# Performance work log

Hardware: AMD Instinct MI355X
Metric: run time of the kernel (lower is better)

Reference implementation:

```python
import jax, jax.numpy as jnp
import numpy as np

KD, KY, KX = 3, 3, 3  # kernel_size from init_kwargs


def setup_inputs() -> dict:
    key = jax.random.key(0)
    x = jax.random.normal(key, (4, 2, 64, 256, 256), dtype=jnp.float32)
    return {"x": x}


def reference(x):
    # x: [B, CH, D, H, W]
    B, CH, D, H, W = x.shape
    pd, py, px = (KD - 1) // 2, (KY - 1) // 2, (KX - 1) // 2
    # replicate padding (torch F.pad mode='replicate' == jnp.pad mode='edge')
    xp = jnp.pad(x, ((0, 0), (0, 0), (pd, pd), (py, py), (px, px)), mode='edge')
    center = (KD * KY * KX) // 2  # flattened center position, excluded from max
    # running max over the 26 non-center neighbors; never materializes the
    # [B, CH, 27, D, H, W] tensor the torch conv3d path creates.
    max_nc = jnp.full(x.shape, -jnp.inf, dtype=x.dtype)
    idx = 0
    for i in range(KD):
        for j in range(KY):
            for k in range(KX):
                if idx != center:
                    shifted = xp[:, :, i:i + D, j:j + H, k:k + W]
                    max_nc = jnp.maximum(max_nc, shifted)
                idx += 1
    mask = x > max_nc  # strict local maximum (excluding self)
    return x * mask.astype(x.dtype)
```

## Files before the change

kernel.cpp:

```cpp
#include <hip/hip_runtime.h>


constexpr int D_   = 64;
constexpr int H_   = 256;
constexpr int W_   = 256;
constexpr int HW_  = H_ * W_;
constexpr int NVOL = 8;
constexpr int DC   = 8;
constexpr int RY   = 8;
constexpr int RS   = RY + 2;
constexpr int NBUF = 3;
constexpr int S    = DC + 2;

__device__ __forceinline__ float f3(float a, float b, float c) {
    return fmaxf(fmaxf(a, b), c);
}

__device__ __forceinline__ void gload16(const float* g, float* l) {
    __builtin_amdgcn_global_load_lds(
        (const __attribute__((address_space(1))) void*)g,
        (__attribute__((address_space(3))) void*)l,
        16, 0, 0);
}

__global__ __launch_bounds__(512, 6)
void nms3d(const float* __restrict__ x, float* __restrict__ out)
{
    __shared__ float lds[NBUF][RS * W_];

    const int tx = threadIdx.x;
    const int ty = threadIdx.y;
    const int h0 = blockIdx.y * RY;
    const int h  = h0 + ty;
    const int n  = blockIdx.z;
    const int z0 = blockIdx.x * DC;
    const int c  = tx << 2;

    const float* __restrict__ base  = x   + (size_t)n * D_ * HW_;
    float* __restrict__       obase = out + (size_t)n * D_ * HW_;

    const int grA = min(max(h0 - 1 + ty, 0), H_ - 1);
    const int grB = min(max(h0 - 1 + RY + ty, 0), H_ - 1);
    const float* gA = base + (size_t)grA * W_ + c;
    const float* gB = base + (size_t)grB * W_ + c;

    auto stage = [&](int t) {
        const int zc = min(max(z0 - 1 + t, 0), D_ - 1);
        const size_t zo = (size_t)zc * HW_;
        float* lp = &lds[t % NBUF][0];
        gload16(gA + zo, lp + ty * W_);
        if (ty < 2) gload16(gB + zo, lp + (RY + ty) * W_);
    };

    stage(0);

    float4 vm9_pp = {0,0,0,0};
    float4 vm9_p  = {0,0,0,0};
    float4 cr8_p  = {0,0,0,0};
    float4 vprev  = {0,0,0,0};

#pragma unroll
    for (int t = 0; t < S; ++t) {
        if (t + 1 < S) {
            stage(t + 1);
            if (ty < 2) asm volatile("s_waitcnt vmcnt(2)" ::: "memory");
            else        asm volatile("s_waitcnt vmcnt(1)" ::: "memory");
        } else {
            asm volatile("s_waitcnt vmcnt(0)" ::: "memory");
        }
        __builtin_amdgcn_s_barrier();
        asm volatile("" ::: "memory");

        const float* p = &lds[t % NBUF][0];
        const float4 a0 = *(const float4*)(p + (ty    ) * W_ + c);
        const float4 b0 = *(const float4*)(p + (ty + 1) * W_ + c);
        const float4 d0 = *(const float4*)(p + (ty + 2) * W_ + c);

        float4 va;
        va.x = fmaxf(a0.x, d0.x); va.y = fmaxf(a0.y, d0.y);
        va.z = fmaxf(a0.z, d0.z); va.w = fmaxf(a0.w, d0.w);

        float vaL = __shfl_up(va.w, 1);   if (tx == 0)  vaL = va.x;
        float vaR = __shfl_down(va.x, 1); if (tx == 63) vaR = va.w;
        float bL  = __shfl_up(b0.w, 1);   if (tx == 0)  bL  = b0.x;
        float bR  = __shfl_down(b0.x, 1); if (tx == 63) bR  = b0.w;

        float4 hv, nb;
        hv.x = f3(vaL, va.x, va.y);  hv.y = f3(va.x, va.y, va.z);
        hv.z = f3(va.y, va.z, va.w); hv.w = f3(va.z, va.w, vaR);
        nb.x = fmaxf(bL,  b0.y);  nb.y = fmaxf(b0.x, b0.z);
        nb.z = fmaxf(b0.y, b0.w); nb.w = fmaxf(b0.z, bR);

        float4 c8, cur;
        c8.x  = fmaxf(hv.x, nb.x); c8.y  = fmaxf(hv.y, nb.y);
        c8.z  = fmaxf(hv.z, nb.z); c8.w  = fmaxf(hv.w, nb.w);
        cur.x = fmaxf(c8.x, b0.x); cur.y = fmaxf(c8.y, b0.y);
        cur.z = fmaxf(c8.z, b0.z); cur.w = fmaxf(c8.w, b0.w);

        if (t >= 2) {
            const int zi = z0 - 1 + t;
            float4 mx, o;
            mx.x = f3(vm9_pp.x, cr8_p.x, cur.x);
            mx.y = f3(vm9_pp.y, cr8_p.y, cur.y);
            mx.z = f3(vm9_pp.z, cr8_p.z, cur.z);
            mx.w = f3(vm9_pp.w, cr8_p.w, cur.w);
            o.x = vprev.x > mx.x ? vprev.x : 0.0f;
            o.y = vprev.y > mx.y ? vprev.y : 0.0f;
            o.z = vprev.z > mx.z ? vprev.z : 0.0f;
            o.w = vprev.w > mx.w ? vprev.w : 0.0f;
            *(float4*)(obase + (size_t)(zi - 1) * HW_ + (size_t)h * W_ + c) = o;
        }
        vm9_pp = vm9_p; vm9_p = cur; cr8_p = c8; vprev = b0;
    }
}

extern "C" void kernel_launch(void* const* d_in, const int* in_sizes, int n_in,
                              void* d_out, int out_size, void* d_ws, size_t ws_size,
                              hipStream_t stream)
{
    const float* x = (const float*)d_in[0];
    float* out = (float*)d_out;
    dim3 block(64, RY, 1);
    dim3 grid(D_ / DC, H_ / RY, NVOL);
    nms3d<<<grid, block, 0, stream>>>(x, out);
}
```

Baseline: 233.4 us.

## Deepen LDS prefetch pipeline, enlarge depth chunk, and flatten block mapping

Each block now processes 16 depth slices instead of 8, which cuts how often halo slices are re-read across blocks. LDS rises to 4 buffers and loads are issued two slices ahead, with per-iteration vmcnt waits adjusted to match. The 3D grid becomes a 1D grid with the volume index varying fastest, and the launch bounds hint rises to 8 blocks. The risks are the hand-counted waitcnt schedule, which must also account for outstanding stores, and fewer blocks overall, which means less parallelism per CU.

```diff
diff --git a/kernel.cpp b/kernel.cpp
--- a/kernel.cpp
+++ b/kernel.cpp
@@ -6,10 +6,10 @@
 constexpr int W_   = 256;
 constexpr int HW_  = H_ * W_;
 constexpr int NVOL = 8;
-constexpr int DC   = 8;
+constexpr int DC   = 16;
 constexpr int RY   = 8;
 constexpr int RS   = RY + 2;
-constexpr int NBUF = 3;
+constexpr int NBUF = 4;
 constexpr int S    = DC + 2;
 
 __device__ __forceinline__ float f3(float a, float b, float c) {
@@ -23,18 +23,34 @@
         16, 0, 0);
 }
 
-__global__ __launch_bounds__(512, 6)
+__device__ __forceinline__ void vmwait(int n) {
+    switch (n) {
+    case 0: asm volatile("s_waitcnt vmcnt(0)" ::: "memory"); break;
+    case 1: asm volatile("s_waitcnt vmcnt(1)" ::: "memory"); break;
+    case 2: asm volatile("s_waitcnt vmcnt(2)" ::: "memory"); break;
+    case 3: asm volatile("s_waitcnt vmcnt(3)" ::: "memory"); break;
+    case 4: asm volatile("s_waitcnt vmcnt(4)" ::: "memory"); break;
+    case 5: asm volatile("s_waitcnt vmcnt(5)" ::: "memory"); break;
+    case 6: asm volatile("s_waitcnt vmcnt(6)" ::: "memory"); break;
+    default: asm volatile("s_waitcnt vmcnt(0)" ::: "memory"); break;
+    }
+}
+
+__global__ __launch_bounds__(512, 8)
 void nms3d(const float* __restrict__ x, float* __restrict__ out)
 {
     __shared__ float lds[NBUF][RS * W_];
 
     const int tx = threadIdx.x;
     const int ty = threadIdx.y;
-    const int h0 = blockIdx.y * RY;
-    const int h  = h0 + ty;
-    const int n  = blockIdx.z;
-    const int z0 = blockIdx.x * DC;
-    const int c  = tx << 2;
+
+    const int bid  = blockIdx.x;
+    const int n    = bid & 7;
+    const int rest = bid >> 3;
+    const int z0   = (rest & 3) * DC;
+    const int h0   = (rest >> 2) * RY;
+    const int h    = h0 + ty;
+    const int c    = tx << 2;
 
     const float* __restrict__ base  = x   + (size_t)n * D_ * HW_;
     float* __restrict__       obase = out + (size_t)n * D_ * HW_;
@@ -47,12 +63,13 @@
     auto stage = [&](int t) {
         const int zc = min(max(z0 - 1 + t, 0), D_ - 1);
         const size_t zo = (size_t)zc * HW_;
-        float* lp = &lds[t % NBUF][0];
+        float* lp = &lds[t & (NBUF - 1)][0];
         gload16(gA + zo, lp + ty * W_);
         if (ty < 2) gload16(gB + zo, lp + (RY + ty) * W_);
     };
 
     stage(0);
+    stage(1);
 
     float4 vm9_pp = {0,0,0,0};
     float4 vm9_p  = {0,0,0,0};
@@ -61,17 +78,20 @@
 
 #pragma unroll
     for (int t = 0; t < S; ++t) {
-        if (t + 1 < S) {
-            stage(t + 1);
-            if (ty < 2) asm volatile("s_waitcnt vmcnt(2)" ::: "memory");
-            else        asm volatile("s_waitcnt vmcnt(1)" ::: "memory");
-        } else {
-            asm volatile("s_waitcnt vmcnt(0)" ::: "memory");
-        }
+        if (t + 2 < S) stage(t + 2);
+
+        int nhi, nlo;
+        if      (t <= 2)     { nhi = 2; nlo = 4; }
+        else if (t == 3)     { nhi = 3; nlo = 5; }
+        else if (t <= S - 3) { nhi = 4; nlo = 6; }
+        else if (t == S - 2) { nhi = 3; nlo = 4; }
+        else                 { nhi = 2; nlo = 2; }
+        vmwait(ty < 2 ? nlo : nhi);
+
         __builtin_amdgcn_s_barrier();
         asm volatile("" ::: "memory");
 
-        const float* p = &lds[t % NBUF][0];
+        const float* p = &lds[t & (NBUF - 1)][0];
         const float4 a0 = *(const float4*)(p + (ty    ) * W_ + c);
         const float4 b0 = *(const float4*)(p + (ty + 1) * W_ + c);
         const float4 d0 = *(const float4*)(p + (ty + 2) * W_ + c);
@@ -121,6 +141,6 @@
     const float* x = (const float*)d_in[0];
     float* out = (float*)d_out;
     dim3 block(64, RY, 1);
-    dim3 grid(D_ / DC, H_ / RY, NVOL);
+    dim3 grid(NVOL * (D_ / DC) * (H_ / RY), 1, 1);
     nms3d<<<grid, block, 0, stream>>>(x, out);
 }
```

New measurement: 239.4 us. +2.6%, slower.
